# Kernel tuning notes

Hardware: AMD Instinct MI355X
Metric: run time of the kernel (lower is better)

The kernel has to match this reference:

```python
import jax, jax.numpy as jnp
import numpy as np

NUM_VOXELS = 1_000_000
N_POINTS = 1_500_000
TOTAL_PROP_PTS = 1_000_000
NUM_PROPOSALS = 2048
IN_CH = 134  # 3 + 3 + 128
M = 16       # backbone output width
BATCH = 8


def setup_inputs() -> dict:
    key = jax.random.key(0)
    k1, k2, k3, k4, k5, k6 = jax.random.split(key, 6)
    voxel_feats = jax.random.normal(k1, (NUM_VOXELS, IN_CH), dtype=jnp.float32)
    W = jax.random.normal(k2, (IN_CH, M), dtype=jnp.float32) * 0.05
    p2v_map = jax.random.randint(k3, (N_POINTS,), 0, NUM_VOXELS, dtype=jnp.int64)
    # column 0: proposal id (unused), column 1: point index into pt_feats
    col1 = jax.random.randint(k4, (TOTAL_PROP_PTS,), 0, N_POINTS, dtype=jnp.int64)
    gt_proposals_idx = jnp.stack([jnp.zeros_like(col1), col1], axis=1)
    interior = jnp.sort(jax.random.randint(k5, (NUM_PROPOSALS - 1,), 0, TOTAL_PROP_PTS, dtype=jnp.int64))
    gt_proposals_offset = jnp.concatenate([
        jnp.zeros((1,), jnp.int64), interior,
        jnp.full((1,), TOTAL_PROP_PTS, jnp.int64)])
    # column 0 is the batch (scene) id
    locs_scaled = jax.random.randint(k6, (N_POINTS, 4), 0, BATCH, dtype=jnp.int32)
    return {
        'voxel_feats': voxel_feats,
        'W': W,
        'p2v_map': p2v_map,
        'gt_proposals_idx': gt_proposals_idx,
        'gt_proposals_offset': gt_proposals_offset,
        'locs_scaled': locs_scaled,
    }


def reference(voxel_feats, W, p2v_map, gt_proposals_idx, gt_proposals_offset, locs_scaled):
    # Stand-in for the Minkowski sparse backbone: pointwise projection + ReLU, 134 -> 16.
    feats = jax.nn.relu(voxel_feats @ W)                 # (V, 16)
    pt_feats = feats[p2v_map]                            # (N, 16) voxel->point gather

    P = gt_proposals_offset.shape[0] - 1
    point_idx = gt_proposals_idx[:, 1]                   # (T,)
    T = point_idx.shape[0]

    # CSR offsets -> segment ids (replaces the Python loop over proposals)
    seg_ids = jnp.searchsorted(gt_proposals_offset, jnp.arange(T), side='right') - 1

    gathered = pt_feats[point_idx]                       # (T, 16) ragged gather
    sums = jax.ops.segment_sum(gathered, seg_ids, num_segments=P)
    counts = jax.ops.segment_sum(jnp.ones((T,), feats.dtype), seg_ids, num_segments=P)
    proposal_feats = sums / jnp.maximum(counts, 1.0)[:, None]   # (P, 16) segment mean

    batch_idxs = locs_scaled[:, 0]                       # (N,) scene ids
    proposals_batchId = batch_idxs[point_idx][gt_proposals_offset[:-1]]  # (P,)
    proposal_objectness_scores = jnp.ones((P,), dtype=bool)
    return proposal_feats, proposals_batchId, proposal_objectness_scores
```

## Files before the change

### kernel.cpp

```cpp
#include <hip/hip_runtime.h>

#define NUM_VOXELS     1000000
#define N_POINTS       1500000
#define TOTAL_PROP_PTS 1000000
#define NUM_PROPOSALS  2048
#define IN_CH          134
#define M_OUT          16

__global__ __launch_bounds__(256, 2) void k_gemm_relu(
    const float* __restrict__ A, const float* __restrict__ W,
    float* __restrict__ feats)
{
    __shared__ float lds[4][64 * 65];
    const int wave = threadIdx.x >> 6;
    const int lane = threadIdx.x & 63;
    const int v0   = blockIdx.x * 256 + wave * 64;
    if (v0 >= NUM_VOXELS) return;

    float* chunk = lds[wave];
    float acc[M_OUT];
#pragma unroll
    for (int c = 0; c < M_OUT; ++c) acc[c] = 0.f;

    for (int kc = 0; kc < IN_CH; kc += 64) {
        const int KC = (IN_CH - kc) >= 64 ? 64 : (IN_CH - kc);
        if (KC == 64) {
            const int half = lane >> 5;
            const int c2   = (lane & 31) * 2;
#pragma unroll 4
            for (int j = 0; j < 32; ++j) {
                const int row = j * 2 + half;
                const float2 val = *(const float2*)(A + (size_t)(v0 + row) * IN_CH + kc + c2);
                chunk[row * 65 + c2]     = val.x;
                chunk[row * 65 + c2 + 1] = val.y;
            }
        } else {
#pragma unroll
            for (int j = 0; j < 6; ++j) {
                const int e   = j * 64 + lane;
                const int row = e / 6;
                const int col = e - row * 6;
                chunk[row * 65 + col] = A[(size_t)(v0 + row) * IN_CH + kc + col];
            }
        }
        const float* wbase = W + kc * M_OUT;
        for (int kk = 0; kk < KC; ++kk) {
            const float a = chunk[lane * 65 + kk];
            const float* wr = wbase + kk * M_OUT;
#pragma unroll
            for (int c = 0; c < M_OUT; ++c) acc[c] = fmaf(a, wr[c], acc[c]);
        }
    }

    float4* orow = (float4*)(feats + (size_t)(v0 + lane) * M_OUT);
#pragma unroll
    for (int q = 0; q < 4; ++q) {
        float4 o;
        o.x = fmaxf(acc[q * 4 + 0], 0.f);
        o.y = fmaxf(acc[q * 4 + 1], 0.f);
        o.z = fmaxf(acc[q * 4 + 2], 0.f);
        o.w = fmaxf(acc[q * 4 + 3], 0.f);
        orow[q] = o;
    }
}

__global__ __launch_bounds__(256) void k_propmean(
    const float* __restrict__ feats,
    const int*   __restrict__ p2v,
    const int*   __restrict__ prop_idx,
    const int*   __restrict__ offsets,
    const int*   __restrict__ locs,
    float*       __restrict__ out)
{
    const int s   = blockIdx.x;
    const int tid = threadIdx.x;
    const int t0  = offsets[s];
    const int t1  = offsets[s + 1];

    float acc[M_OUT];
#pragma unroll
    for (int c = 0; c < M_OUT; ++c) acc[c] = 0.f;

    for (int t = t0 + tid; t < t1; t += 256) {
        const int p = prop_idx[2 * t + 1];
        const int v = p2v[p];
        const float4* fp = (const float4*)(feats + (size_t)v * M_OUT);
        const float4 f0 = fp[0], f1 = fp[1], f2 = fp[2], f3 = fp[3];
        acc[0]  += f0.x; acc[1]  += f0.y; acc[2]  += f0.z; acc[3]  += f0.w;
        acc[4]  += f1.x; acc[5]  += f1.y; acc[6]  += f1.z; acc[7]  += f1.w;
        acc[8]  += f2.x; acc[9]  += f2.y; acc[10] += f2.z; acc[11] += f2.w;
        acc[12] += f3.x; acc[13] += f3.y; acc[14] += f3.z; acc[15] += f3.w;
    }

#pragma unroll
    for (int c = 0; c < M_OUT; ++c) {
#pragma unroll
        for (int off = 32; off > 0; off >>= 1)
            acc[c] += __shfl_down(acc[c], off, 64);
    }

    __shared__ float red[4][M_OUT];
    const int lane = tid & 63, wv = tid >> 6;
    if (lane == 0) {
#pragma unroll
        for (int c = 0; c < M_OUT; ++c) red[wv][c] = acc[c];
    }
    __syncthreads();

    if (tid < M_OUT) {
        const float sum = red[0][tid] + red[1][tid] + red[2][tid] + red[3][tid];
        const float cnt = (float)(t1 - t0);
        out[s * M_OUT + tid] = sum / fmaxf(cnt, 1.f);
    }
    if (tid == 0) {
        const int p = prop_idx[2 * t0 + 1];
        out[NUM_PROPOSALS * M_OUT + s]                 = (float)locs[4 * p];
        out[NUM_PROPOSALS * M_OUT + NUM_PROPOSALS + s] = 1.0f;
    }
}

extern "C" void kernel_launch(void* const* d_in, const int* in_sizes, int n_in,
                              void* d_out, int out_size, void* d_ws, size_t ws_size,
                              hipStream_t stream)
{
    const float* A    = (const float*)d_in[0];
    const float* W    = (const float*)d_in[1];
    const int*   p2v  = (const int*)  d_in[2];
    const int*   pidx = (const int*)  d_in[3];
    const int*   offs = (const int*)  d_in[4];
    const int*   locs = (const int*)  d_in[5];
    float*       out  = (float*)      d_out;
    float*       feats = (float*)     d_ws;

    k_gemm_relu<<<(NUM_VOXELS + 255) / 256, 256, 0, stream>>>(A, W, feats);
    k_propmean<<<NUM_PROPOSALS, 256, 0, stream>>>(feats, p2v, pidx, offs, locs, out);
}
```

Before: 792.3 us.

## Compute GEMM rows only for referenced voxels and store features in bf16

Two pre-passes zero and then set a per-voxel byte flag for every voxel reached through the proposal point indices. The GEMM kernel skips global loads and output stores for unflagged rows, cutting HBM traffic for the roughly half of voxels never used, though the FMA loop still runs for every row. Backbone features are now stored as packed bf16, which halves the scattered gather traffic in the proposal-mean kernel. This costs two extra launches, a flag buffer and lower feature precision.

```diff
diff --git a/kernel.cpp b/kernel.cpp
--- a/kernel.cpp
+++ b/kernel.cpp
@@ -7,15 +7,42 @@
 #define IN_CH          134
 #define M_OUT          16
 
+typedef unsigned int  uint;
+typedef unsigned short ushort;
+
+__device__ __forceinline__ ushort f2bf(float f) {
+    uint u = __float_as_uint(f);
+    uint r = (u + 0x7FFFu + ((u >> 16) & 1u)) >> 16;
+    return (ushort)r;
+}
+
+__global__ void k_zero_flags(uint* __restrict__ flags4) {
+    int i = blockIdx.x * 256 + threadIdx.x;
+    if (i < NUM_VOXELS / 4) flags4[i] = 0;
+}
+
+__global__ void k_set_flags(const int* __restrict__ prop_idx,
+                            const int* __restrict__ p2v,
+                            unsigned char* __restrict__ flags) {
+    int t = blockIdx.x * 256 + threadIdx.x;
+    if (t < TOTAL_PROP_PTS) {
+        int p = prop_idx[2 * t + 1];
+        flags[p2v[p]] = 1;
+    }
+}
+
 __global__ __launch_bounds__(256, 2) void k_gemm_relu(
     const float* __restrict__ A, const float* __restrict__ W,
-    float* __restrict__ feats)
+    const unsigned char* __restrict__ flags,
+    uint* __restrict__ featsb)
 {
     __shared__ float lds[4][64 * 65];
     const int wave = threadIdx.x >> 6;
     const int lane = threadIdx.x & 63;
     const int v0   = blockIdx.x * 256 + wave * 64;
     if (v0 >= NUM_VOXELS) return;
+
+    const int myflag = flags[v0 + lane];
 
     float* chunk = lds[wave];
     float acc[M_OUT];
@@ -27,12 +54,15 @@
         if (KC == 64) {
             const int half = lane >> 5;
             const int c2   = (lane & 31) * 2;
-#pragma unroll 4
+#pragma unroll 8
             for (int j = 0; j < 32; ++j) {
                 const int row = j * 2 + half;
-                const float2 val = *(const float2*)(A + (size_t)(v0 + row) * IN_CH + kc + c2);
-                chunk[row * 65 + c2]     = val.x;
-                chunk[row * 65 + c2 + 1] = val.y;
+                const int rf  = __shfl(myflag, row, 64);
+                if (rf) {
+                    const float2 val = *(const float2*)(A + (size_t)(v0 + row) * IN_CH + kc + c2);
+                    chunk[row * 65 + c2]     = val.x;
+                    chunk[row * 65 + c2 + 1] = val.y;
+                }
             }
         } else {
 #pragma unroll
@@ -40,7 +70,8 @@
                 const int e   = j * 64 + lane;
                 const int row = e / 6;
                 const int col = e - row * 6;
-                chunk[row * 65 + col] = A[(size_t)(v0 + row) * IN_CH + kc + col];
+                const int rf  = __shfl(myflag, row, 64);
+                if (rf) chunk[row * 65 + col] = A[(size_t)(v0 + row) * IN_CH + kc + col];
             }
         }
         const float* wbase = W + kc * M_OUT;
@@ -52,20 +83,22 @@
         }
     }
 
-    float4* orow = (float4*)(feats + (size_t)(v0 + lane) * M_OUT);
+    if (myflag) {
+        uint u[8];
 #pragma unroll
-    for (int q = 0; q < 4; ++q) {
-        float4 o;
-        o.x = fmaxf(acc[q * 4 + 0], 0.f);
-        o.y = fmaxf(acc[q * 4 + 1], 0.f);
-        o.z = fmaxf(acc[q * 4 + 2], 0.f);
-        o.w = fmaxf(acc[q * 4 + 3], 0.f);
-        orow[q] = o;
+        for (int i = 0; i < 8; ++i) {
+            const float lo = fmaxf(acc[2 * i],     0.f);
+            const float hi = fmaxf(acc[2 * i + 1], 0.f);
+            u[i] = (uint)f2bf(lo) | ((uint)f2bf(hi) << 16);
+        }
+        uint4* orow = (uint4*)(featsb + (size_t)(v0 + lane) * 8);
+        orow[0] = make_uint4(u[0], u[1], u[2], u[3]);
+        orow[1] = make_uint4(u[4], u[5], u[6], u[7]);
     }
 }
 
 __global__ __launch_bounds__(256) void k_propmean(
-    const float* __restrict__ feats,
+    const uint*  __restrict__ featsb,
     const int*   __restrict__ p2v,
     const int*   __restrict__ prop_idx,
     const int*   __restrict__ offsets,
@@ -84,12 +117,14 @@
     for (int t = t0 + tid; t < t1; t += 256) {
         const int p = prop_idx[2 * t + 1];
         const int v = p2v[p];
-        const float4* fp = (const float4*)(feats + (size_t)v * M_OUT);
-        const float4 f0 = fp[0], f1 = fp[1], f2 = fp[2], f3 = fp[3];
-        acc[0]  += f0.x; acc[1]  += f0.y; acc[2]  += f0.z; acc[3]  += f0.w;
-        acc[4]  += f1.x; acc[5]  += f1.y; acc[6]  += f1.z; acc[7]  += f1.w;
-        acc[8]  += f2.x; acc[9]  += f2.y; acc[10] += f2.z; acc[11] += f2.w;
-        acc[12] += f3.x; acc[13] += f3.y; acc[14] += f3.z; acc[15] += f3.w;
+        const uint4* fp = (const uint4*)(featsb + (size_t)v * 8);
+        const uint4 q0 = fp[0], q1 = fp[1];
+        const uint u[8] = {q0.x, q0.y, q0.z, q0.w, q1.x, q1.y, q1.z, q1.w};
+#pragma unroll
+        for (int i = 0; i < 8; ++i) {
+            acc[2 * i]     += __uint_as_float(u[i] << 16);
+            acc[2 * i + 1] += __uint_as_float(u[i] & 0xFFFF0000u);
+        }
     }
 
 #pragma unroll
@@ -130,8 +165,12 @@
     const int*   offs = (const int*)  d_in[4];
     const int*   locs = (const int*)  d_in[5];
     float*       out  = (float*)      d_out;
-    float*       feats = (float*)     d_ws;
 
-    k_gemm_relu<<<(NUM_VOXELS + 255) / 256, 256, 0, stream>>>(A, W, feats);
-    k_propmean<<<NUM_PROPOSALS, 256, 0, stream>>>(feats, p2v, pidx, offs, locs, out);
+    uint*          featsb = (uint*)d_ws;
+    unsigned char* flags  = (unsigned char*)d_ws + (size_t)NUM_VOXELS * 32;
+
+    k_zero_flags<<<(NUM_VOXELS / 4 + 255) / 256, 256, 0, stream>>>((uint*)flags);
+    k_set_flags<<<(TOTAL_PROP_PTS + 255) / 256, 256, 0, stream>>>(pidx, p2v, flags);
+    k_gemm_relu<<<(NUM_VOXELS + 255) / 256, 256, 0, stream>>>(A, W, flags, featsb);
+    k_propmean<<<NUM_PROPOSALS, 256, 0, stream>>>(featsb, p2v, pidx, offs, locs, out);
 }
```

After: 940.1 us. 1.19x slower.
